# Optimization experiments

Hardware: AMD Instinct MI355X
Metric: run time of the kernel (lower is better)

Reference implementation:

```python
import jax, jax.numpy as jnp
import numpy as np

V = 25000
E = 100000
NODE_IN = 74
EDGE_IN = 12
OUT = 64
EHID = 128
NUM_STEPS = 6


def setup_inputs() -> dict:
    key = jax.random.key(0)
    ks = jax.random.split(key, 12)
    s = 0.05
    node_feats = jax.random.normal(ks[0], (V, NODE_IN), dtype=jnp.float32)
    edge_feats = jax.random.normal(ks[1], (E, EDGE_IN), dtype=jnp.float32)
    src = jax.random.randint(ks[2], (E,), 0, V)
    dst = jax.random.randint(ks[3], (E,), 0, V)
    # project_node_feats: Linear(node_in, out)
    Wp = jax.random.normal(ks[4], (NODE_IN, OUT), dtype=jnp.float32) * s
    bp = jnp.zeros((OUT,), dtype=jnp.float32)
    # edge network: Linear(edge_in, ehid) -> ReLU -> Linear(ehid, out*out)
    We1 = jax.random.normal(ks[5], (EDGE_IN, EHID), dtype=jnp.float32) * s
    be1 = jnp.zeros((EHID,), dtype=jnp.float32)
    We2 = jax.random.normal(ks[6], (EHID, OUT * OUT), dtype=jnp.float32) * s
    be2 = jnp.zeros((OUT * OUT,), dtype=jnp.float32)
    # NNConv output bias
    bias = jnp.zeros((OUT,), dtype=jnp.float32)
    return {
        "node_feats": node_feats, "edge_feats": edge_feats,
        "src": src, "dst": dst,
        "Wp": Wp, "bp": bp,
        "We1": We1, "be1": be1, "We2": We2, "be2": be2,
        "bias": bias,
    }


def reference(node_feats, edge_feats, src, dst, Wp, bp, We1, be1, We2, be2, bias):
    # project node features
    h = jax.nn.relu(node_feats @ Wp + bp)  # [V, OUT]
    # per-edge weight matrices (same every step -> hoist out of loop)
    ew = jax.nn.relu(edge_feats @ We1 + be1) @ We2 + be2  # [E, OUT*OUT]
    ew = ew.reshape(E, OUT, OUT)
    for _ in range(NUM_STEPS):
        # gather src node feats, batched matvec, scatter-sum to dst
        msg = jnp.einsum('ei,eio->eo', h[src], ew)  # [E, OUT]
        agg = jax.ops.segment_sum(msg, dst, num_segments=V)  # [V, OUT]
        h = jax.nn.relu(agg + bias)
    return h
```

## Files before the change

kernel.cpp:

```cpp
#include <hip/hip_runtime.h>
#include <hip/hip_bf16.h>

#define Vn 25000
#define En 100000
#define NODE_IN 74
#define EDGE_IN 12
#define OUTD 64
#define EHID 128
#define NUM_STEPS 6

#define HPAD 68

typedef __attribute__((ext_vector_type(8))) _Float16 half8;
typedef __attribute__((ext_vector_type(4))) float floatx4;

__global__ void proj_kernel(const float* __restrict__ node,
                            const float* __restrict__ Wp,
                            const float* __restrict__ bp,
                            float* __restrict__ h) {
  __shared__ float nf[NODE_IN];
  int v = blockIdx.x;
  int o = threadIdx.x;
  for (int i = o; i < NODE_IN; i += 64) nf[i] = node[(size_t)v * NODE_IN + i];
  __syncthreads();
  float acc = bp[o];
  for (int i = 0; i < NODE_IN; ++i) acc = fmaf(nf[i], Wp[i * OUTD + o], acc);
  h[(size_t)v * OUTD + o] = fmaxf(acc, 0.0f);
}

__global__ void edge_kernel(const float* __restrict__ ef,
                            const float* __restrict__ We1,
                            const float* __restrict__ be1,
                            _Float16* __restrict__ f) {
  __shared__ float es[EDGE_IN];
  int e = blockIdx.x;
  int k = threadIdx.x;
  if (k < EDGE_IN) es[k] = ef[(size_t)e * EDGE_IN + k];
  __syncthreads();
  float acc = be1[k];
  for (int j = 0; j < EDGE_IN; ++j) acc = fmaf(es[j], We1[j * EHID + k], acc);
  f[(size_t)e * EHID + k] = (_Float16)fmaxf(acc, 0.0f);
}

__global__ void w2r_kernel(const float* __restrict__ We2,
                           _Float16* __restrict__ w2s) {
  int g = blockIdx.x * 256 + threadIdx.x;
  int j = g & 7;
  int quad = (g >> 3) & 3;
  int l15 = (g >> 5) & 15;
  int c = (g >> 9) & 3;
  int step = g >> 11;
  int s = step & 3;
  int i = step >> 2;
  int k = s * 32 + quad * 8 + j;
  int col = i * 64 + c * 16 + l15;
  w2s[g] = (_Float16)We2[(size_t)k * (OUTD * OUTD) + col];
}

__global__ __launch_bounds__(256, 2) void msg_kernel(
    const float* __restrict__ h,
    const _Float16* __restrict__ f,
    const _Float16* __restrict__ w2s,
    const int* __restrict__ src,
    const int* __restrict__ dst,
    const float* __restrict__ be2,
    float* __restrict__ agg) {
  __shared__ __align__(16) float smem[8192];
  __shared__ int s_dst[64];

  const int tid = threadIdx.x;
  const int wv = tid >> 6;
  const int lane = tid & 63;
  const int quad = lane >> 4;
  const int l15 = lane & 15;
  const int e0 = blockIdx.x * 64;

  if (tid < 64) {
    int e = e0 + tid;
    s_dst[tid] = (e < En) ? dst[e] : -1;
  }
  {
    int e = tid & 63;
    int ib = tid >> 6;
    int eg = e0 + e;
    int sv = (eg < En) ? src[eg] : 0;
    const float4* hp = reinterpret_cast<const float4*>(h + (size_t)sv * OUTD + ib * 16);
    for (int c = 0; c < 4; ++c) {
      float4 val = hp[c];
      int i4 = ib * 16 + c * 4;
      smem[(i4 + 0) * HPAD + e] = val.x;
      smem[(i4 + 1) * HPAD + e] = val.y;
      smem[(i4 + 2) * HPAD + e] = val.z;
      smem[(i4 + 3) * HPAD + e] = val.w;
    }
  }
  __syncthreads();

  half8 afr[4][4];
#pragma unroll
  for (int t = 0; t < 4; ++t) {
    int e = e0 + t * 16 + l15;
    if (e >= En) e = En - 1;
    const _Float16* fr = f + (size_t)e * EHID + quad * 8;
#pragma unroll
    for (int s = 0; s < 4; ++s)
      afr[t][s] = *reinterpret_cast<const half8*>(fr + s * 32);
  }

  const _Float16* w2l = w2s + l15 * 32 + quad * 8;

#define LOADB4(B, STEP)                                                     \
  {                                                                         \
    const _Float16* p_ = w2l + (size_t)(STEP) * 2048;                       \
    B[0] = *reinterpret_cast<const half8*>(p_);                             \
    B[1] = *reinterpret_cast<const half8*>(p_ + 512);                       \
    B[2] = *reinterpret_cast<const half8*>(p_ + 1024);                      \
    B[3] = *reinterpret_cast<const half8*>(p_ + 1536);                      \
  }

  floatx4 acc[4][4];
  const floatx4 zero4 = (floatx4){0.f, 0.f, 0.f, 0.f};
#pragma unroll
  for (int t = 0; t < 4; ++t)
#pragma unroll
    for (int c = 0; c < 4; ++c) acc[t][c] = zero4;

  const int ibase = wv * 16;
  const int sbase = ibase * 4;
  const int smax = sbase + 63;

  half8 B0[4], B1[4], B2[4], B3[4];
  LOADB4(B0, sbase);
  LOADB4(B1, sbase + 1);
  LOADB4(B2, sbase + 2);

#define SSTEP(SS, USE, PF)                                                    \
  {                                                                           \
    int ps_ = sb + (SS) + 3;                                                  \
    if (ps_ > smax) ps_ = smax;       \
    LOADB4(PF, ps_);                                                          \
    _Pragma("unroll") for (int t = 0; t < 4; ++t) {                           \
      half8 as = afr[t][SS] * hb[t];                                          \
      acc[t][0] = __builtin_amdgcn_mfma_f32_16x16x32_f16(as, USE[0], acc[t][0], 0, 0, 0); \
      acc[t][1] = __builtin_amdgcn_mfma_f32_16x16x32_f16(as, USE[1], acc[t][1], 0, 0, 0); \
      acc[t][2] = __builtin_amdgcn_mfma_f32_16x16x32_f16(as, USE[2], acc[t][2], 0, 0, 0); \
      acc[t][3] = __builtin_amdgcn_mfma_f32_16x16x32_f16(as, USE[3], acc[t][3], 0, 0, 0); \
    }                                                                         \
  }

  for (int ii = 0; ii < 16; ++ii) {
    int iv = ibase + ii;
    int sb = iv * 4;
    half8 hb[4];
#pragma unroll
    for (int t = 0; t < 4; ++t) {
      _Float16 hf = (_Float16)smem[iv * HPAD + t * 16 + l15];
      hb[t] = (half8){hf, hf, hf, hf, hf, hf, hf, hf};
    }
    SSTEP(0, B0, B3);
    SSTEP(1, B1, B0);
    SSTEP(2, B2, B1);
    SSTEP(3, B3, B2);
  }

  if (wv == 0) {
#pragma unroll
    for (int s = 0; s < 2; ++s) {
      half8 b2f[4];
#pragma unroll
      for (int c = 0; c < 4; ++c) {
        half8 v;
#pragma unroll
        for (int j = 0; j < 8; ++j)
          v[j] = (_Float16)be2[(s * 32 + quad * 8 + j) * 64 + c * 16 + l15];
        b2f[c] = v;
      }
#pragma unroll
      for (int t = 0; t < 4; ++t) {
        half8 ha;
#pragma unroll
        for (int j = 0; j < 8; ++j)
          ha[j] = (_Float16)smem[(s * 32 + quad * 8 + j) * HPAD + t * 16 + l15];
#pragma unroll
        for (int c = 0; c < 4; ++c)
          acc[t][c] = __builtin_amdgcn_mfma_f32_16x16x32_f16(ha, b2f[c], acc[t][c], 0, 0, 0);
      }
    }
  }

  floatx4* scv = reinterpret_cast<floatx4*>(smem);

#define ST1(TG)                                                           \
  _Pragma("unroll") for (int c = 0; c < 4; ++c)                           \
      scv[wv * 512 + (((TG) & 1) * 4 + c) * 64 + lane] = acc[TG][c];
#define LD1(TK)                                                           \
  _Pragma("unroll") for (int c = 0; c < 4; ++c)                           \
      acc[TK][c] += scv[(wv ^ 1) * 512 + (((TK) & 1) * 4 + c) * 64 + lane];
#define ST2(TG)                                                           \
  _Pragma("unroll") for (int c = 0; c < 4; ++c)                           \
      scv[wv * 512 + c * 64 + lane] = acc[TG][c];
#define LD2(TK)                                                           \
  _Pragma("unroll") for (int c = 0; c < 4; ++c)                           \
      acc[TK][c] += scv[(wv ^ 2) * 512 + c * 64 + lane];
#define SCAT(TF)                                                          \
  {                                                                       \
    int rb = (TF) * 16 + quad * 4;                                        \
    _Pragma("unroll") for (int c = 0; c < 4; ++c) {                       \
      int col = c * 16 + l15;                                             \
      _Pragma("unroll") for (int r = 0; r < 4; ++r) {                     \
        int d = s_dst[rb + r];                                            \
        if (d >= 0) atomicAdd(&agg[(size_t)d * OUTD + col], acc[TF][c][r]); \
      }                                                                   \
    }                                                                     \
  }

  __syncthreads();
  if ((wv & 1) == 0) { ST1(2); ST1(3); } else { ST1(0); ST1(1); }
  __syncthreads();
  if ((wv & 1) == 0) { LD1(0); LD1(1); } else { LD1(2); LD1(3); }
  __syncthreads();
  if (wv == 0) { ST2(1); } else if (wv == 1) { ST2(3); }
  else if (wv == 2) { ST2(0); } else { ST2(2); }
  __syncthreads();
  if (wv == 0) { LD2(0); SCAT(0); }
  else if (wv == 1) { LD2(2); SCAT(2); }
  else if (wv == 2) { LD2(1); SCAT(1); }
  else { LD2(3); SCAT(3); }
}

__global__ void update_kernel(float* __restrict__ agg,
                              const float* __restrict__ bias,
                              float* __restrict__ hout,
                              float* __restrict__ dout, int last) {
  int g = blockIdx.x * 256 + threadIdx.x;
  if (g >= Vn * OUTD) return;
  float v = agg[g];
  agg[g] = 0.0f;
  float r = fmaxf(v + bias[g & 63], 0.0f);
  hout[g] = r;
  if (last) dout[g] = r;
}

extern "C" void kernel_launch(void* const* d_in, const int* in_sizes, int n_in,
                              void* d_out, int out_size, void* d_ws, size_t ws_size,
                              hipStream_t stream) {
  const float* node = (const float*)d_in[0];
  const float* edge = (const float*)d_in[1];
  const int* src = (const int*)d_in[2];
  const int* dst = (const int*)d_in[3];
  const float* Wp   = (const float*)d_in[4];
  const float* bp   = (const float*)d_in[5];
  const float* We1  = (const float*)d_in[6];
  const float* be1  = (const float*)d_in[7];
  const float* We2  = (const float*)d_in[8];
  const float* be2  = (const float*)d_in[9];
  const float* bias = (const float*)d_in[10];
  float* out = (float*)d_out;

  char* ws = (char*)d_ws;
  float* agg = (float*)(ws);
  float* h_a = (float*)(ws + 6400000);
  float* h_b = (float*)(ws + 12800000);
  _Float16* f   = (_Float16*)(ws + 19200000);
  _Float16* w2s = (_Float16*)(ws + 44800000);

  hipMemsetAsync(agg, 0, (size_t)Vn * OUTD * sizeof(float), stream);
  proj_kernel<<<Vn, 64, 0, stream>>>(node, Wp, bp, h_a);
  edge_kernel<<<En, 128, 0, stream>>>(edge, We1, be1, f);
  w2r_kernel<<<(OUTD * OUTD * EHID) / 256, 256, 0, stream>>>(We2, w2s);

  float* hin = h_a;
  float* hout = h_b;
  for (int s = 0; s < NUM_STEPS; ++s) {
    msg_kernel<<<(En + 63) / 64, 256, 0, stream>>>(hin, f, w2s, src, dst, be2, agg);
    update_kernel<<<(Vn * OUTD + 255) / 256, 256, 0, stream>>>(
        agg, bias, hout, out, s == NUM_STEPS - 1);
    float* t = hin; hin = hout; hout = t;
  }
}
```

Baseline: 1.003 ms.

## Stage edge-network weights through LDS ring via direct global-to-LDS loads

Replaces the register-prefetched global loads of the swizzled We2 fragments with a per-wave two-slot LDS ring filled by global_load_lds, paced by explicit vmcnt/lgkmcnt waits. The w2s layout gets an XOR swizzle so the LDS fragment reads avoid bank conflicts. Dropping the four-deep B register buffers lets launch bounds rise from 2 to 3 blocks per CU. The cost is a larger shared-memory footprint, which could itself limit occupancy, plus hand-written wait counts that must match the ordering of the asynchronous loads.

```diff
diff --git a/kernel.cpp b/kernel.cpp
--- a/kernel.cpp
+++ b/kernel.cpp
@@ -54,10 +54,17 @@
   int i = step >> 2;
   int k = s * 32 + quad * 8 + j;
   int col = i * 64 + c * 16 + l15;
-  w2s[g] = (_Float16)We2[(size_t)k * (OUTD * OUTD) + col];
-}
-
-__global__ __launch_bounds__(256, 2) void msg_kernel(
+  int eidx = g & 2047;
+  int estore = eidx ^ (((eidx >> 6) & 3) << 3);
+  w2s[((size_t)step << 11) | estore] = (_Float16)We2[(size_t)k * (OUTD * OUTD) + col];
+}
+
+#define GLOAD_LDS(gp, lp)                                                     \
+  __builtin_amdgcn_global_load_lds(                                           \
+      (const __attribute__((address_space(1))) void*)(gp),                    \
+      (__attribute__((address_space(3))) void*)(lp), 16, 0, 0)
+
+__global__ __launch_bounds__(256, 3) void msg_kernel(
     const float* __restrict__ h,
     const _Float16* __restrict__ f,
     const _Float16* __restrict__ w2s,
@@ -65,7 +72,7 @@
     const int* __restrict__ dst,
     const float* __restrict__ be2,
     float* __restrict__ agg) {
-  __shared__ __align__(16) float smem[8192];
+  __shared__ __align__(16) float smem[12544];
   __shared__ int s_dst[64];
 
   const int tid = threadIdx.x;
@@ -107,17 +114,6 @@
       afr[t][s] = *reinterpret_cast<const half8*>(fr + s * 32);
   }
 
-  const _Float16* w2l = w2s + l15 * 32 + quad * 8;
-
-#define LOADB4(B, STEP)                                                     \
-  {                                                                         \
-    const _Float16* p_ = w2l + (size_t)(STEP) * 2048;                       \
-    B[0] = *reinterpret_cast<const half8*>(p_);                             \
-    B[1] = *reinterpret_cast<const half8*>(p_ + 512);                       \
-    B[2] = *reinterpret_cast<const half8*>(p_ + 1024);                      \
-    B[3] = *reinterpret_cast<const half8*>(p_ + 1536);                      \
-  }
-
   floatx4 acc[4][4];
   const floatx4 zero4 = (floatx4){0.f, 0.f, 0.f, 0.f};
 #pragma unroll
@@ -126,41 +122,71 @@
     for (int c = 0; c < 4; ++c) acc[t][c] = zero4;
 
   const int ibase = wv * 16;
-  const int sbase = ibase * 4;
-  const int smax = sbase + 63;
-
-  half8 B0[4], B1[4], B2[4], B3[4];
-  LOADB4(B0, sbase);
-  LOADB4(B1, sbase + 1);
-  LOADB4(B2, sbase + 2);
-
-#define SSTEP(SS, USE, PF)                                                    \
+
+  char* ring = (char*)smem + 4352 * 4 + wv * 8192;
+  const char* w2b = (const char*)w2s;
+  const int roff = l15 * 64 + ((quad ^ ((l15 >> 1) & 3)) << 4);
+  const char* slot0p = ring + roff;
+  const char* slot1p = ring + 4096 + roff;
+
+#define STAGE(GS, SLOT)                                                       \
   {                                                                           \
-    int ps_ = sb + (SS) + 3;                                                  \
-    if (ps_ > smax) ps_ = smax;       \
-    LOADB4(PF, ps_);                                                          \
+    const char* gp_ = w2b + (size_t)(GS) * 4096 + lane * 16;                  \
+    char* lp_ = ring + (SLOT) * 4096;                                         \
+    GLOAD_LDS(gp_, lp_);                                                      \
+    GLOAD_LDS(gp_ + 1024, lp_ + 1024);                                        \
+    GLOAD_LDS(gp_ + 2048, lp_ + 2048);                                        \
+    GLOAD_LDS(gp_ + 3072, lp_ + 3072);                                        \
+  }
+
+#define VM4 asm volatile("s_waitcnt vmcnt(4)" ::: "memory")
+#define VM0 asm volatile("s_waitcnt vmcnt(0)" ::: "memory")
+#define LGKM0 asm volatile("s_waitcnt lgkmcnt(0)" ::: "memory")
+
+#define KSTEP(SS, SLOTP, SLOT, WAIT, DOSTAGE, IV)                             \
+  {                                                                           \
+    WAIT;                                                                     \
+    half8 b0_ = *reinterpret_cast<const half8*>(SLOTP);                       \
+    half8 b1_ = *reinterpret_cast<const half8*>(SLOTP + 1024);                \
+    half8 b2_ = *reinterpret_cast<const half8*>(SLOTP + 2048);                \
+    half8 b3_ = *reinterpret_cast<const half8*>(SLOTP + 3072);                \
+    LGKM0;                                                                    \
+    __builtin_amdgcn_sched_barrier(0);                                        \
+    if (DOSTAGE) STAGE(((IV) << 2) + (SS) + 2, SLOT);                         \
     _Pragma("unroll") for (int t = 0; t < 4; ++t) {                           \
       half8 as = afr[t][SS] * hb[t];                                          \
-      acc[t][0] = __builtin_amdgcn_mfma_f32_16x16x32_f16(as, USE[0], acc[t][0], 0, 0, 0); \
-      acc[t][1] = __builtin_amdgcn_mfma_f32_16x16x32_f16(as, USE[1], acc[t][1], 0, 0, 0); \
-      acc[t][2] = __builtin_amdgcn_mfma_f32_16x16x32_f16(as, USE[2], acc[t][2], 0, 0, 0); \
-      acc[t][3] = __builtin_amdgcn_mfma_f32_16x16x32_f16(as, USE[3], acc[t][3], 0, 0, 0); \
+      acc[t][0] = __builtin_amdgcn_mfma_f32_16x16x32_f16(as, b0_, acc[t][0], 0, 0, 0); \
+      acc[t][1] = __builtin_amdgcn_mfma_f32_16x16x32_f16(as, b1_, acc[t][1], 0, 0, 0); \
+      acc[t][2] = __builtin_amdgcn_mfma_f32_16x16x32_f16(as, b2_, acc[t][2], 0, 0, 0); \
+      acc[t][3] = __builtin_amdgcn_mfma_f32_16x16x32_f16(as, b3_, acc[t][3], 0, 0, 0); \
     }                                                                         \
   }
 
-  for (int ii = 0; ii < 16; ++ii) {
+#define BUILD_HB(IV)                                                          \
+  half8 hb[4];                                                                \
+  _Pragma("unroll") for (int t = 0; t < 4; ++t) {                             \
+    _Float16 hf = (_Float16)smem[(IV) * HPAD + t * 16 + l15];                 \
+    hb[t] = (half8){hf, hf, hf, hf, hf, hf, hf, hf};                          \
+  }
+
+  STAGE(ibase * 4, 0);
+  STAGE(ibase * 4 + 1, 1);
+
+  for (int ii = 0; ii < 15; ++ii) {
     int iv = ibase + ii;
-    int sb = iv * 4;
-    half8 hb[4];
-#pragma unroll
-    for (int t = 0; t < 4; ++t) {
-      _Float16 hf = (_Float16)smem[iv * HPAD + t * 16 + l15];
-      hb[t] = (half8){hf, hf, hf, hf, hf, hf, hf, hf};
-    }
-    SSTEP(0, B0, B3);
-    SSTEP(1, B1, B0);
-    SSTEP(2, B2, B1);
-    SSTEP(3, B3, B2);
+    BUILD_HB(iv);
+    KSTEP(0, slot0p, 0, VM4, 1, iv);
+    KSTEP(1, slot1p, 1, VM4, 1, iv);
+    KSTEP(2, slot0p, 0, VM4, 1, iv);
+    KSTEP(3, slot1p, 1, VM4, 1, iv);
+  }
+  {
+    int iv = ibase + 15;
+    BUILD_HB(iv);
+    KSTEP(0, slot0p, 0, VM4, 1, iv);
+    KSTEP(1, slot1p, 1, VM4, 1, iv);
+    KSTEP(2, slot0p, 0, VM4, 0, iv);
+    KSTEP(3, slot1p, 1, VM0, 0, iv);
   }
 
   if (wv == 0) {
```

New measurement: 810.1 us. 1.24x faster.
